# Kernel optimization log

Measured on AMD Instinct MI355X. Metric: run time of the kernel, lower is better.

The kernel has to match this reference:

```python
import jax, jax.numpy as jnp
import numpy as np

BN_INV = 1.0 / np.sqrt(1.0 + 1e-5)  # eval-mode BatchNorm1d with running_mean=0, running_var=1


def _lin_bn_relu(x, W, g, b):
    # Linear(no bias) -> BN(eval) -> ReLU
    return jax.nn.relu((x @ W.T) * (g * BN_INV) + b)


def setup_inputs() -> dict:
    key = jax.random.key(0)
    ks = jax.random.split(key, 24)
    B, P, N, C, H, OUT = 8, 1024, 20, 32, 256, 256
    s = 0.05
    inp = {
        "polylines": jax.random.normal(ks[0], (B, P, N, C), dtype=jnp.float32),
        "polylines_mask": jax.random.randint(ks[1], (B, P, N), 0, 2) > 0,
        # pre_mlps: [Lin(C->H,no bias)+BN+ReLU] x2, Lin(H->H, bias)
        "pre_w0": jax.random.normal(ks[2], (H, C), dtype=jnp.float32) * s,
        "pre_g0": jnp.ones((H,), jnp.float32),
        "pre_b0": jnp.zeros((H,), jnp.float32),
        "pre_w1": jax.random.normal(ks[3], (H, H), dtype=jnp.float32) * s,
        "pre_g1": jnp.ones((H,), jnp.float32),
        "pre_b1": jnp.zeros((H,), jnp.float32),
        "pre_w2": jax.random.normal(ks[4], (H, H), dtype=jnp.float32) * s,
        "pre_bias2": jnp.zeros((H,), jnp.float32),
        # mlps: c_in=2H -> [H,H,H]
        "mlp_w0": jax.random.normal(ks[5], (H, 2 * H), dtype=jnp.float32) * s,
        "mlp_g0": jnp.ones((H,), jnp.float32),
        "mlp_b0": jnp.zeros((H,), jnp.float32),
        "mlp_w1": jax.random.normal(ks[6], (H, H), dtype=jnp.float32) * s,
        "mlp_g1": jnp.ones((H,), jnp.float32),
        "mlp_b1": jnp.zeros((H,), jnp.float32),
        "mlp_w2": jax.random.normal(ks[7], (H, H), dtype=jnp.float32) * s,
        "mlp_bias2": jnp.zeros((H,), jnp.float32),
        # out_mlps (without_norm): Lin(H->H,bias)+ReLU, Lin(H->OUT,bias)
        "out_w0": jax.random.normal(ks[8], (H, H), dtype=jnp.float32) * s,
        "out_b0": jnp.zeros((H,), jnp.float32),
        "out_w1": jax.random.normal(ks[9], (OUT, H), dtype=jnp.float32) * s,
        "out_b1": jnp.zeros((OUT,), jnp.float32),
    }
    return inp


def reference(polylines, polylines_mask,
              pre_w0, pre_g0, pre_b0, pre_w1, pre_g1, pre_b1, pre_w2, pre_bias2,
              mlp_w0, mlp_g0, mlp_b0, mlp_w1, mlp_g1, mlp_b1, mlp_w2, mlp_bias2,
              out_w0, out_b0, out_w1, out_b1):
    # gather->MLP->zero-scatter is equivalent to dense MLP followed by mask-zeroing
    # (all per-point ops are elementwise / last-dim matmuls).
    m = polylines_mask[..., None].astype(polylines.dtype)  # (B,P,N,1)

    x = _lin_bn_relu(polylines, pre_w0, pre_g0, pre_b0)
    x = _lin_bn_relu(x, pre_w1, pre_g1, pre_b1)
    x = (x @ pre_w2.T + pre_bias2) * m                      # (B,P,N,H) zero at invalid

    pooled = x.max(axis=2)                                  # (B,P,H) max over zero-filled buffer
    x = jnp.concatenate(
        [x, jnp.broadcast_to(pooled[:, :, None, :], x.shape)], axis=-1)  # (B,P,N,2H)

    x = _lin_bn_relu(x, mlp_w0, mlp_g0, mlp_b0)
    x = _lin_bn_relu(x, mlp_w1, mlp_g1, mlp_b1)
    x = (x @ mlp_w2.T + mlp_bias2) * m                      # (B,P,N,H)

    buf = x.max(axis=2)                                     # (B,P,H)

    valid = jnp.any(polylines_mask, axis=-1)                # sum(mask)>0
    y = jax.nn.relu(buf @ out_w0.T + out_b0)
    y = (y @ out_w1.T + out_b1) * valid[..., None].astype(buf.dtype)  # (B,P,OUT)
    return y
```

## Files before the change

kernel.cpp:

```cpp
#include <hip/hip_runtime.h>
#include <stdint.h>
#include <stddef.h>

typedef __bf16 bf16;
typedef __bf16 bf16x4 __attribute__((ext_vector_type(4)));
typedef __bf16 bf16x8 __attribute__((ext_vector_type(8)));
typedef float f32x4 __attribute__((ext_vector_type(4)));
typedef float f32x16 __attribute__((ext_vector_type(16)));

#define BNI 0.9999950000374996f
#define NROW 240
#define NPOLYB 12
#define TOTROW 163840
#define NPOLY 8192
#define NBLK 683

#define AADDR(r, ch) ((r)*256 + ((((ch) ^ ((r)&31)))<<3))

#define OFF_ACT  0
#define OFF_WB0  122880
#define OFF_T2   155648
#define OFF_VAL  161792
#define LDS_TOTAL 161840

#define WS_PRE_W0 0
#define WS_PRE_W1 8192
#define WS_PRE_W2 73728
#define WS_MLP_W0 139264
#define WS_MLP_W1 270336
#define WS_MLP_W2 335872
#define WS_OUT_W0 401408
#define WS_OUT_W1 466944

__device__ __forceinline__ bf16 f2b(float f){
  unsigned int i = __builtin_bit_cast(unsigned int, f);
  unsigned int r = i + 0x7fffu + ((i >> 16) & 1u);
  unsigned short h = (unsigned short)(r >> 16);
  return __builtin_bit_cast(bf16, h);
}
__device__ __forceinline__ float b2f(bf16 x){
  unsigned short u = __builtin_bit_cast(unsigned short, x);
  union { unsigned int i; float f; } v; v.i = ((unsigned int)u) << 16; return v.f;
}
__device__ __forceinline__ bf16x8 ld8f(const float* p, float sc){
  f32x4 a = *(const f32x4*)p;
  f32x4 b = *(const f32x4*)(p + 4);
  bf16x8 r;
  #pragma unroll
  for (int j = 0; j < 4; ++j){ r[j] = f2b(a[j]*sc); r[4+j] = f2b(b[j]*sc); }
  return r;
}

__global__ __launch_bounds__(256)
void prep_kernel(const float* s0, const float* s1, const float* s2, const float* s3,
                 const float* s4, const float* s5, const float* s6, const float* s7,
                 const float* g0, const float* g1, const float* g3, const float* g4,
                 bf16* dst)
{
  const int offs[8] = {WS_PRE_W0, WS_PRE_W1, WS_PRE_W2, WS_MLP_W0,
                       WS_MLP_W1, WS_MLP_W2, WS_OUT_W0, WS_OUT_W1};
  const int sz[8]   = {8192, 65536, 65536, 131072, 65536, 65536, 65536, 65536};
  const int ld[8]   = {32, 256, 256, 512, 256, 256, 256, 256};
  int r = blockIdx.y;
  const float* src = s0;
  if (r == 1) src = s1; else if (r == 2) src = s2; else if (r == 3) src = s3;
  else if (r == 4) src = s4; else if (r == 5) src = s5; else if (r == 6) src = s6;
  else if (r == 7) src = s7;
  const float* gp = (r==0)?g0:(r==1)?g1:(r==3)?g3:(r==4)?g4:nullptr;
  int i = (blockIdx.x*256 + threadIdx.x)*8;
  if (i < sz[r]){
    float sc = gp ? gp[i/ld[r]]*BNI : 1.0f;
    *(bf16x8*)&dst[offs[r] + i] = ld8f(src + i, sc);
  }
}

__device__ __forceinline__ void stageAsyncG(const bf16* W, int ldK, int tile, int kh,
                                            bf16* buf, int wg, int lane){
  int id = wg*64 + lane;
  int fr = id >> 4, kcd = id & 15;
  int kcs = kcd ^ (fr & 15);
  const bf16* gp = W + (size_t)(tile*32 + fr)*ldK + kh*128 + kcs*8;
  bf16* l = buf + (size_t)(wg*64)*8;
  __builtin_amdgcn_global_load_lds(
      (const __attribute__((address_space(1))) void*)gp,
      (__attribute__((address_space(3))) void*)l,
      16, 0, 0);
}

template<int RELU, int MASK, int ADDT2>
__device__ __forceinline__ void epiT(
    const f32x16& acc, int nt, int row, int poly, float mk, bool valid,
    bf16* sAct, const bf16* sT2, const float* bptr, int hi)
{
  #pragma unroll
  for (int q2 = 0; q2 < 4; ++q2){
    int f0 = nt*32 + 8*q2 + 4*hi;
    f32x4 bb = *(const f32x4*)(bptr + f0);
    bf16x4 tv = {};
    if (ADDT2) tv = *(const bf16x4*)&sT2[poly*256 + f0];
    bf16x4 o;
    #pragma unroll
    for (int j = 0; j < 4; ++j){
      float v = acc[4*q2 + j];
      if (ADDT2) v += b2f(tv[j]);
      v += bb[j];
      if (RELU) v = fmaxf(v, 0.0f);
      if (MASK) v *= mk;
      o[j] = f2b(v);
    }
    if (valid)
      *(bf16x4*)&sAct[row*256 + (((nt*4 + q2) ^ (row & 31))<<3) + 4*hi] = o;
  }
}

template<int RELU, int MASK, int ADDT2>
__device__ __forceinline__ void layerT16(
    bf16* sAct, bf16* wbase, const bf16* sT2,
    const bf16* W, int ldK, const float* bptr,
    const int* maskp, int blk, int g, int wg, int row, int rowc,
    int lane32, int hi, int lane)
{
  bf16x8 B[16];
  #pragma unroll
  for (int t = 0; t < 16; ++t)
    B[t] = *(const bf16x8*)&sAct[AADDR(rowc, 2*t + hi)];

  float mk = 1.0f;
  if (MASK){
    int gr = blk*NROW + row;
    mk = (row < NROW && gr < TOTROW && maskp[gr]) ? 1.0f : 0.0f;
  }
  const int poly = rowc/20;
  const bool valid = row < NROW;
  bf16* bufA = wbase + (size_t)(2*g)*4096;
  bf16* bufB = bufA + 4096;

  stageAsyncG(W, ldK, g*4, 0, bufA, wg, lane);
  __syncthreads();
  #pragma unroll 1
  for (int p = 0; p < 4; ++p){
    f32x16 acc;
    stageAsyncG(W, ldK, g*4 + p, 1, bufB, wg, lane);
    {
      bf16x8 wf[8];
      const bf16* base = bufA + lane32*128;
      #pragma unroll
      for (int t = 0; t < 8; ++t)
        wf[t] = *(const bf16x8*)(base + (((2*t + hi) ^ (lane32 & 15))<<3));
      #pragma unroll
      for (int j = 0; j < 16; ++j) acc[j] = 0.0f;
      #pragma unroll
      for (int t = 0; t < 8; ++t)
        acc = __builtin_amdgcn_mfma_f32_32x32x16_bf16(wf[t], B[t], acc, 0, 0, 0);
    }
    __syncthreads();
    if (p < 3) stageAsyncG(W, ldK, g*4 + p + 1, 0, bufA, wg, lane);
    {
      bf16x8 wf[8];
      const bf16* base = bufB + lane32*128;
      #pragma unroll
      for (int t = 0; t < 8; ++t)
        wf[t] = *(const bf16x8*)(base + (((2*t + hi) ^ (lane32 & 15))<<3));
      #pragma unroll
      for (int t = 0; t < 8; ++t)
        acc = __builtin_amdgcn_mfma_f32_32x32x16_bf16(wf[t], B[8 + t], acc, 0, 0, 0);
      epiT<RELU,MASK,ADDT2>(acc, g*4 + p, row, poly, mk, valid, sAct, sT2, bptr, hi);
    }
    __syncthreads();
  }
}

__device__ __forceinline__ void poolT(const bf16* sAct, bf16* sPool, int tid){
  if (tid < 384){
    int poly = tid >> 5, c = tid & 31;
    float m[8];
    bf16x8 v0 = *(const bf16x8*)&sAct[AADDR(poly*20, c)];
    #pragma unroll
    for (int j = 0; j < 8; ++j) m[j] = b2f(v0[j]);
    for (int r = 1; r < 20; ++r){
      bf16x8 v = *(const bf16x8*)&sAct[AADDR(poly*20 + r, c)];
      #pragma unroll
      for (int j = 0; j < 8; ++j) m[j] = fmaxf(m[j], b2f(v[j]));
    }
    bf16x8 o;
    #pragma unroll
    for (int j = 0; j < 8; ++j) o[j] = f2b(m[j]);
    *(bf16x8*)&sPool[AADDR(poly, c)] = o;
  }
}

__global__ __launch_bounds__(1024) __attribute__((amdgpu_waves_per_eu(4, 4)))
void traj_kernel(const float* __restrict__ poly, const int* __restrict__ maskp,
                 const float* pre_b0, const float* pre_b1, const float* pre_bias2,
                 const float* mlp_b0, const float* mlp_b1, const float* mlp_bias2,
                 const float* out_b0, const float* out_b1,
                 const bf16* __restrict__ ws,
                 float* __restrict__ outp)
{
  extern __shared__ char smem[];
  bf16*  sAct   = (bf16*)(smem + OFF_ACT);
  bf16*  wbase  = (bf16*)(smem + OFF_WB0);
  bf16*  sT2    = (bf16*)(smem + OFF_T2);
  float* sValid = (float*)(smem + OFF_VAL);
  bf16*  sPool  = wbase;
  bf16*  sY     = sAct;

  const int tid = threadIdx.x;
  const int w = tid >> 6, L = tid & 63, lane32 = L & 31, hi = L >> 5;
  const int g = w >> 3, wg = w & 7;
  const int row  = wg*32 + lane32;
  const int rowc = row < NROW ? row : NROW - 1;
  const int blk = blockIdx.x;

  const bf16* pw0 = ws + WS_PRE_W0;
  const bf16* pw1 = ws + WS_PRE_W1;
  const bf16* pw2 = ws + WS_PRE_W2;
  const bf16* mw0 = ws + WS_MLP_W0;
  const bf16* mw1 = ws + WS_MLP_W1;
  const bf16* mw2 = ws + WS_MLP_W2;
  const bf16* ow0 = ws + WS_OUT_W0;
  const bf16* ow1 = ws + WS_OUT_W1;

  if (tid < 960){
    int r = tid >> 2, c = tid & 3;
    int grow = blk*NROW + r;
    bf16x8 v = {};
    if (grow < TOTROW) v = ld8f(poly + (size_t)grow*32 + c*8, 1.0f);
    *(bf16x8*)&sAct[AADDR(r, c)] = v;
  }
  __syncthreads();
  if (tid < NPOLYB){
    float v = 0.0f;
    #pragma unroll
    for (int r = 0; r < 20; ++r){
      int gg = blk*NROW + tid*20 + r;
      if (gg < TOTROW && maskp[gg]) v = 1.0f;
    }
    sValid[tid] = v;
  }

  {
    bf16x8 B0 = *(const bf16x8*)&sAct[AADDR(rowc, hi)];
    bf16x8 B1 = *(const bf16x8*)&sAct[AADDR(rowc, 2 + hi)];
    __syncthreads();
    #pragma unroll 1
    for (int ntl = 0; ntl < 4; ++ntl){
      int nt = g*4 + ntl;
      const bf16* p = pw0 + (size_t)(nt*32 + lane32)*32 + 8*hi;
      bf16x8 w0 = *(const bf16x8*)p;
      bf16x8 w1 = *(const bf16x8*)(p + 16);
      f32x16 acc = {};
      acc = __builtin_amdgcn_mfma_f32_32x32x16_bf16(w0, B0, acc, 0, 0, 0);
      acc = __builtin_amdgcn_mfma_f32_32x32x16_bf16(w1, B1, acc, 0, 0, 0);
      epiT<1,0,0>(acc, nt, row, 0, 1.0f, row < NROW, sAct, sT2, pre_b0, hi);
    }
  }
  __syncthreads();

  layerT16<1,0,0>(sAct, wbase, sT2, pw1, 256, pre_b1,    maskp, blk, g, wg, row, rowc, lane32, hi, L);
  layerT16<0,1,0>(sAct, wbase, sT2, pw2, 256, pre_bias2, maskp, blk, g, wg, row, rowc, lane32, hi, L);

  poolT(sAct, sPool, tid);
  __syncthreads();

  if (w < 8){
    bf16x8 Bp[16];
    #pragma unroll
    for (int t = 0; t < 16; ++t)
      Bp[t] = *(const bf16x8*)&sPool[AADDR((lane32 < NPOLYB ? lane32 : 0), 2*t + hi)];
    int nt = w;
    const bf16* p = mw0 + (size_t)(nt*32 + lane32)*512 + 256 + 8*hi;
    f32x16 acc = {};
    #pragma unroll
    for (int t = 0; t < 16; ++t){
      bf16x8 wf = *(const bf16x8*)(p + 16*t);
      acc = __builtin_amdgcn_mfma_f32_32x32x16_bf16(wf, Bp[t], acc, 0, 0, 0);
    }
    if (lane32 < NPOLYB){
      #pragma unroll
      for (int q2 = 0; q2 < 4; ++q2){
        int f0 = nt*32 + 8*q2 + 4*hi;
        bf16x4 o;
        #pragma unroll
        for (int j = 0; j < 4; ++j) o[j] = f2b(acc[4*q2 + j]);
        *(bf16x4*)&sT2[lane32*256 + f0] = o;
      }
    }
  }
  __syncthreads();

  layerT16<1,0,1>(sAct, wbase, sT2, mw0, 512, mlp_b0,    maskp, blk, g, wg, row, rowc, lane32, hi, L);
  layerT16<1,0,0>(sAct, wbase, sT2, mw1, 256, mlp_b1,    maskp, blk, g, wg, row, rowc, lane32, hi, L);
  layerT16<0,1,0>(sAct, wbase, sT2, mw2, 256, mlp_bias2, maskp, blk, g, wg, row, rowc, lane32, hi, L);

  poolT(sAct, sPool, tid);
  __syncthreads();

  if (w < 8){
    bf16x8 Bp[16];
    #pragma unroll
    for (int t = 0; t < 16; ++t)
      Bp[t] = *(const bf16x8*)&sPool[AADDR((lane32 < NPOLYB ? lane32 : 0), 2*t + hi)];
    int nt = w;
    const bf16* p = ow0 + (size_t)(nt*32 + lane32)*256 + 8*hi;
    f32x16 acc = {};
    #pragma unroll
    for (int t = 0; t < 16; ++t){
      bf16x8 wf = *(const bf16x8*)(p + 16*t);
      acc = __builtin_amdgcn_mfma_f32_32x32x16_bf16(wf, Bp[t], acc, 0, 0, 0);
    }
    if (lane32 < NPOLYB){
      #pragma unroll
      for (int q2 = 0; q2 < 4; ++q2){
        int f0 = nt*32 + 8*q2 + 4*hi;
        f32x4 bb = *(const f32x4*)(out_b0 + f0);
        bf16x4 o;
        #pragma unroll
        for (int j = 0; j < 4; ++j) o[j] = f2b(fmaxf(acc[4*q2 + j] + bb[j], 0.0f));
        *(bf16x4*)&sY[lane32*256 + (((nt*4 + q2) ^ (lane32 & 31))<<3) + 4*hi] = o;
      }
    }
  }
  __syncthreads();

  if (w < 8){
    bf16x8 By[16];
    #pragma unroll
    for (int t = 0; t < 16; ++t)
      By[t] = *(const bf16x8*)&sY[AADDR((lane32 < NPOLYB ? lane32 : 0), 2*t + hi)];
    int gp = blk*NPOLYB + lane32;
    float vd = (lane32 < NPOLYB) ? sValid[lane32] : 0.0f;
    int nt = w;
    const bf16* p = ow1 + (size_t)(nt*32 + lane32)*256 + 8*hi;
    f32x16 acc = {};
    #pragma unroll
    for (int t = 0; t < 16; ++t){
      bf16x8 wf = *(const bf16x8*)(p + 16*t);
      acc = __builtin_amdgcn_mfma_f32_32x32x16_bf16(wf, By[t], acc, 0, 0, 0);
    }
    if (lane32 < NPOLYB && gp < NPOLY){
      #pragma unroll
      for (int q2 = 0; q2 < 4; ++q2){
        int f0 = nt*32 + 8*q2 + 4*hi;
        f32x4 bb = *(const f32x4*)(out_b1 + f0);
        f32x4 o;
        #pragma unroll
        for (int j = 0; j < 4; ++j) o[j] = (acc[4*q2 + j] + bb[j]) * vd;
        *(f32x4*)&outp[(size_t)gp*256 + f0] = o;
      }
    }
  }
}

extern "C" void kernel_launch(void* const* d_in, const int* in_sizes, int n_in,
                              void* d_out, int out_size, void* d_ws, size_t ws_size,
                              hipStream_t stream)
{
  const float* poly      = (const float*)d_in[0];
  const int*   maskp     = (const int*)  d_in[1];
  const float* pre_w0    = (const float*)d_in[2];
  const float* pre_g0    = (const float*)d_in[3];
  const float* pre_b0    = (const float*)d_in[4];
  const float* pre_w1    = (const float*)d_in[5];
  const float* pre_g1    = (const float*)d_in[6];
  const float* pre_b1    = (const float*)d_in[7];
  const float* pre_w2    = (const float*)d_in[8];
  const float* pre_bias2 = (const float*)d_in[9];
  const float* mlp_w0    = (const float*)d_in[10];
  const float* mlp_g0    = (const float*)d_in[11];
  const float* mlp_b0    = (const float*)d_in[12];
  const float* mlp_w1    = (const float*)d_in[13];
  const float* mlp_g1    = (const float*)d_in[14];
  const float* mlp_b1    = (const float*)d_in[15];
  const float* mlp_w2    = (const float*)d_in[16];
  const float* mlp_bias2 = (const float*)d_in[17];
  const float* out_w0    = (const float*)d_in[18];
  const float* out_b0    = (const float*)d_in[19];
  const float* out_w1    = (const float*)d_in[20];
  const float* out_b1    = (const float*)d_in[21];

  bf16* ws = (bf16*)d_ws;

  (void)hipFuncSetAttribute((const void*)&traj_kernel,
                            hipFuncAttributeMaxDynamicSharedMemorySize, LDS_TOTAL);

  prep_kernel<<<dim3(64, 8), dim3(256), 0, stream>>>(
      pre_w0, pre_w1, pre_w2, mlp_w0, mlp_w1, mlp_w2, out_w0, out_w1,
      pre_g0, pre_g1, mlp_g0, mlp_g1, ws);

  traj_kernel<<<dim3(NBLK), dim3(1024), LDS_TOTAL, stream>>>(
      poly, maskp,
      pre_b0, pre_b1, pre_bias2,
      mlp_b0, mlp_b1, mlp_bias2,
      out_b0, out_b1,
      ws, (float*)d_out);
}
```

Measured before the change: 326.0 us.

## Halve block to 512 threads and compute two row tiles per wave

The main kernel drops from 1024 to 512 threads per block, and each wave now owns two 32-row tiles instead of one. Each weight fragment read from LDS feeds two MFMAs, one per row tile. The weight staging, input loading and pooling/output stages are remapped to the smaller thread count. This halves LDS weight-fragment reads per row and the number of waves per CU. It doubles per-wave register use for activations and accumulators, so there is less wave-level parallelism to hide latency.

After: 324.7 us. Within noise of the previous version (-0.4%).

```diff
diff --git a/kernel.cpp b/kernel.cpp
--- a/kernel.cpp
+++ b/kernel.cpp
@@ -74,17 +74,20 @@
   }
 }
 
-__device__ __forceinline__ void stageAsyncG(const bf16* W, int ldK, int tile, int kh,
-                                            bf16* buf, int wg, int lane){
-  int id = wg*64 + lane;
-  int fr = id >> 4, kcd = id & 15;
-  int kcs = kcd ^ (fr & 15);
-  const bf16* gp = W + (size_t)(tile*32 + fr)*ldK + kh*128 + kcs*8;
-  bf16* l = buf + (size_t)(wg*64)*8;
-  __builtin_amdgcn_global_load_lds(
-      (const __attribute__((address_space(1))) void*)gp,
-      (__attribute__((address_space(3))) void*)l,
-      16, 0, 0);
+__device__ __forceinline__ void stageAsyncG2(const bf16* W, int ldK, int tile, int kh,
+                                             bf16* buf, int rp, int lane){
+  #pragma unroll
+  for (int i = 0; i < 2; ++i){
+    int id = rp*128 + i*64 + lane;
+    int fr = id >> 4, kcd = id & 15;
+    int kcs = kcd ^ (fr & 15);
+    const bf16* gsrc = W + (size_t)(tile*32 + fr)*ldK + kh*128 + kcs*8;
+    bf16* l = buf + (size_t)(rp*128 + i*64)*8;
+    __builtin_amdgcn_global_load_lds(
+        (const __attribute__((address_space(1))) void*)gsrc,
+        (__attribute__((address_space(3))) void*)l,
+        16, 0, 0);
+  }
 }
 
 template<int RELU, int MASK, int ADDT2>
@@ -114,57 +117,58 @@
 }
 
 template<int RELU, int MASK, int ADDT2>
-__device__ __forceinline__ void layerT16(
+__device__ __forceinline__ void layerR2(
     bf16* sAct, bf16* wbase, const bf16* sT2,
     const bf16* W, int ldK, const float* bptr,
-    const int* maskp, int blk, int g, int wg, int row, int rowc,
-    int lane32, int hi, int lane)
+    const int* maskp, int blk, int g, int rp, int row0, int row1,
+    int rowc0, int rowc1, int lane32, int hi, int lane)
 {
-  bf16x8 B[16];
+  bf16x8 B0[16], B1[16];
   #pragma unroll
-  for (int t = 0; t < 16; ++t)
-    B[t] = *(const bf16x8*)&sAct[AADDR(rowc, 2*t + hi)];
-
-  float mk = 1.0f;
+  for (int t = 0; t < 16; ++t){
+    B0[t] = *(const bf16x8*)&sAct[AADDR(rowc0, 2*t + hi)];
+    B1[t] = *(const bf16x8*)&sAct[AADDR(rowc1, 2*t + hi)];
+  }
+  float mk0 = 1.0f, mk1 = 1.0f;
   if (MASK){
-    int gr = blk*NROW + row;
-    mk = (row < NROW && gr < TOTROW && maskp[gr]) ? 1.0f : 0.0f;
-  }
-  const int poly = rowc/20;
-  const bool valid = row < NROW;
+    int g0 = blk*NROW + row0, g1 = blk*NROW + row1;
+    mk0 = (row0 < NROW && g0 < TOTROW && maskp[g0]) ? 1.0f : 0.0f;
+    mk1 = (row1 < NROW && g1 < TOTROW && maskp[g1]) ? 1.0f : 0.0f;
+  }
+  const int poly0 = rowc0/20, poly1 = rowc1/20;
+  const bool valid0 = row0 < NROW, valid1 = row1 < NROW;
   bf16* bufA = wbase + (size_t)(2*g)*4096;
   bf16* bufB = bufA + 4096;
 
-  stageAsyncG(W, ldK, g*4, 0, bufA, wg, lane);
+  stageAsyncG2(W, ldK, g*4, 0, bufA, rp, lane);
   __syncthreads();
   #pragma unroll 1
   for (int p = 0; p < 4; ++p){
-    f32x16 acc;
-    stageAsyncG(W, ldK, g*4 + p, 1, bufB, wg, lane);
+    f32x16 acc0, acc1;
+    stageAsyncG2(W, ldK, g*4 + p, 1, bufB, rp, lane);
     {
-      bf16x8 wf[8];
       const bf16* base = bufA + lane32*128;
       #pragma unroll
-      for (int t = 0; t < 8; ++t)
-        wf[t] = *(const bf16x8*)(base + (((2*t + hi) ^ (lane32 & 15))<<3));
-      #pragma unroll
-      for (int j = 0; j < 16; ++j) acc[j] = 0.0f;
-      #pragma unroll
-      for (int t = 0; t < 8; ++t)
-        acc = __builtin_amdgcn_mfma_f32_32x32x16_bf16(wf[t], B[t], acc, 0, 0, 0);
+      for (int j = 0; j < 16; ++j){ acc0[j] = 0.0f; acc1[j] = 0.0f; }
+      #pragma unroll
+      for (int t = 0; t < 8; ++t){
+        bf16x8 wf = *(const bf16x8*)(base + (((2*t + hi) ^ (lane32 & 15))<<3));
+        acc0 = __builtin_amdgcn_mfma_f32_32x32x16_bf16(wf, B0[t], acc0, 0, 0, 0);
+        acc1 = __builtin_amdgcn_mfma_f32_32x32x16_bf16(wf, B1[t], acc1, 0, 0, 0);
+      }
     }
     __syncthreads();
-    if (p < 3) stageAsyncG(W, ldK, g*4 + p + 1, 0, bufA, wg, lane);
+    if (p < 3) stageAsyncG2(W, ldK, g*4 + p + 1, 0, bufA, rp, lane);
     {
-      bf16x8 wf[8];
       const bf16* base = bufB + lane32*128;
       #pragma unroll
-      for (int t = 0; t < 8; ++t)
-        wf[t] = *(const bf16x8*)(base + (((2*t + hi) ^ (lane32 & 15))<<3));
-      #pragma unroll
-      for (int t = 0; t < 8; ++t)
-        acc = __builtin_amdgcn_mfma_f32_32x32x16_bf16(wf[t], B[8 + t], acc, 0, 0, 0);
-      epiT<RELU,MASK,ADDT2>(acc, g*4 + p, row, poly, mk, valid, sAct, sT2, bptr, hi);
+      for (int t = 0; t < 8; ++t){
+        bf16x8 wf = *(const bf16x8*)(base + (((2*t + hi) ^ (lane32 & 15))<<3));
+        acc0 = __builtin_amdgcn_mfma_f32_32x32x16_bf16(wf, B0[8 + t], acc0, 0, 0, 0);
+        acc1 = __builtin_amdgcn_mfma_f32_32x32x16_bf16(wf, B1[8 + t], acc1, 0, 0, 0);
+      }
+      epiT<RELU,MASK,ADDT2>(acc0, g*4 + p, row0, poly0, mk0, valid0, sAct, sT2, bptr, hi);
+      epiT<RELU,MASK,ADDT2>(acc1, g*4 + p, row1, poly1, mk1, valid1, sAct, sT2, bptr, hi);
     }
     __syncthreads();
   }
@@ -189,7 +193,7 @@
   }
 }
 
-__global__ __launch_bounds__(1024) __attribute__((amdgpu_waves_per_eu(4, 4)))
+__global__ __launch_bounds__(512) __attribute__((amdgpu_waves_per_eu(2, 2)))
 void traj_kernel(const float* __restrict__ poly, const int* __restrict__ maskp,
                  const float* pre_b0, const float* pre_b1, const float* pre_bias2,
                  const float* mlp_b0, const float* mlp_b1, const float* mlp_bias2,
@@ -207,9 +211,11 @@
 
   const int tid = threadIdx.x;
   const int w = tid >> 6, L = tid & 63, lane32 = L & 31, hi = L >> 5;
-  const int g = w >> 3, wg = w & 7;
-  const int row  = wg*32 + lane32;
-  const int rowc = row < NROW ? row : NROW - 1;
+  const int g = w >> 2, rp = w & 3;
+  const int row0 = rp*64 + lane32;
+  const int row1 = row0 + 32;
+  const int rowc0 = row0 < NROW ? row0 : NROW - 1;
+  const int rowc1 = row1 < NROW ? row1 : NROW - 1;
   const int blk = blockIdx.x;
 
   const bf16* pw0 = ws + WS_PRE_W0;
@@ -221,12 +227,16 @@
   const bf16* ow0 = ws + WS_OUT_W0;
   const bf16* ow1 = ws + WS_OUT_W1;
 
-  if (tid < 960){
-    int r = tid >> 2, c = tid & 3;
-    int grow = blk*NROW + r;
-    bf16x8 v = {};
-    if (grow < TOTROW) v = ld8f(poly + (size_t)grow*32 + c*8, 1.0f);
-    *(bf16x8*)&sAct[AADDR(r, c)] = v;
+  #pragma unroll
+  for (int i = 0; i < 2; ++i){
+    int id = tid + 512*i;
+    if (id < 960){
+      int r = id >> 2, c = id & 3;
+      int grow = blk*NROW + r;
+      bf16x8 v = {};
+      if (grow < TOTROW) v = ld8f(poly + (size_t)grow*32 + c*8, 1.0f);
+      *(bf16x8*)&sAct[AADDR(r, c)] = v;
+    }
   }
   __syncthreads();
   if (tid < NPOLYB){
@@ -240,8 +250,10 @@
   }
 
   {
-    bf16x8 B0 = *(const bf16x8*)&sAct[AADDR(rowc, hi)];
-    bf16x8 B1 = *(const bf16x8*)&sAct[AADDR(rowc, 2 + hi)];
+    bf16x8 B00 = *(const bf16x8*)&sAct[AADDR(rowc0, hi)];
+    bf16x8 B01 = *(const bf16x8*)&sAct[AADDR(rowc0, 2 + hi)];
+    bf16x8 B10 = *(const bf16x8*)&sAct[AADDR(rowc1, hi)];
+    bf16x8 B11 = *(const bf16x8*)&sAct[AADDR(rowc1, 2 + hi)];
     __syncthreads();
     #pragma unroll 1
     for (int ntl = 0; ntl < 4; ++ntl){
@@ -249,21 +261,24 @@
       const bf16* p = pw0 + (size_t)(nt*32 + lane32)*32 + 8*hi;
       bf16x8 w0 = *(const bf16x8*)p;
       bf16x8 w1 = *(const bf16x8*)(p + 16);
-      f32x16 acc = {};
-      acc = __builtin_amdgcn_mfma_f32_32x32x16_bf16(w0, B0, acc, 0, 0, 0);
-      acc = __builtin_amdgcn_mfma_f32_32x32x16_bf16(w1, B1, acc, 0, 0, 0);
-      epiT<1,0,0>(acc, nt, row, 0, 1.0f, row < NROW, sAct, sT2, pre_b0, hi);
-    }
-  }
-  __syncthreads();
-
-  layerT16<1,0,0>(sAct, wbase, sT2, pw1, 256, pre_b1,    maskp, blk, g, wg, row, rowc, lane32, hi, L);
-  layerT16<0,1,0>(sAct, wbase, sT2, pw2, 256, pre_bias2, maskp, blk, g, wg, row, rowc, lane32, hi, L);
+      f32x16 acc0 = {}, acc1 = {};
+      acc0 = __builtin_amdgcn_mfma_f32_32x32x16_bf16(w0, B00, acc0, 0, 0, 0);
+      acc0 = __builtin_amdgcn_mfma_f32_32x32x16_bf16(w1, B01, acc0, 0, 0, 0);
+      acc1 = __builtin_amdgcn_mfma_f32_32x32x16_bf16(w0, B10, acc1, 0, 0, 0);
+      acc1 = __builtin_amdgcn_mfma_f32_32x32x16_bf16(w1, B11, acc1, 0, 0, 0);
+      epiT<1,0,0>(acc0, nt, row0, 0, 1.0f, row0 < NROW, sAct, sT2, pre_b0, hi);
+      epiT<1,0,0>(acc1, nt, row1, 0, 1.0f, row1 < NROW, sAct, sT2, pre_b0, hi);
+    }
+  }
+  __syncthreads();
+
+  layerR2<1,0,0>(sAct, wbase, sT2, pw1, 256, pre_b1,    maskp, blk, g, rp, row0, row1, rowc0, rowc1, lane32, hi, L);
+  layerR2<0,1,0>(sAct, wbase, sT2, pw2, 256, pre_bias2, maskp, blk, g, rp, row0, row1, rowc0, rowc1, lane32, hi, L);
 
   poolT(sAct, sPool, tid);
   __syncthreads();
 
-  if (w < 8){
+  {
     bf16x8 Bp[16];
     #pragma unroll
     for (int t = 0; t < 16; ++t)
@@ -289,14 +304,14 @@
   }
   __syncthreads();
 
-  layerT16<1,0,1>(sAct, wbase, sT2, mw0, 512, mlp_b0,    maskp, blk, g, wg, row, rowc, lane32, hi, L);
-  layerT16<1,0,0>(sAct, wbase, sT2, mw1, 256, mlp_b1,    maskp, blk, g, wg, row, rowc, lane32, hi, L);
-  layerT16<0,1,0>(sAct, wbase, sT2, mw2, 256, mlp_bias2, maskp, blk, g, wg, row, rowc, lane32, hi, L);
+  layerR2<1,0,1>(sAct, wbase, sT2, mw0, 512, mlp_b0,    maskp, blk, g, rp, row0, row1, rowc0, rowc1, lane32, hi, L);
+  layerR2<1,0,0>(sAct, wbase, sT2, mw1, 256, mlp_b1,    maskp, blk, g, rp, row0, row1, rowc0, rowc1, lane32, hi, L);
+  layerR2<0,1,0>(sAct, wbase, sT2, mw2, 256, mlp_bias2, maskp, blk, g, rp, row0, row1, rowc0, rowc1, lane32, hi, L);
 
   poolT(sAct, sPool, tid);
   __syncthreads();
 
-  if (w < 8){
+  {
     bf16x8 Bp[16];
     #pragma unroll
     for (int t = 0; t < 16; ++t)
@@ -323,7 +338,7 @@
   }
   __syncthreads();
 
-  if (w < 8){
+  {
     bf16x8 By[16];
     #pragma unroll
     for (int t = 0; t < 16; ++t)
@@ -388,7 +403,7 @@
       pre_w0, pre_w1, pre_w2, mlp_w0, mlp_w1, mlp_w2, out_w0, out_w1,
       pre_g0, pre_g1, mlp_g0, mlp_g1, ws);
 
-  traj_kernel<<<dim3(NBLK), dim3(1024), LDS_TOTAL, stream>>>(
+  traj_kernel<<<dim3(NBLK), dim3(512), LDS_TOTAL, stream>>>(
       poly, maskp,
       pre_b0, pre_b1, pre_bias2,
       mlp_b0, mlp_b1, mlp_bias2,
```
